# Kernel optimization log

Hardware: AMD Instinct MI355X
Metric: run time of the kernel (lower is better)

## Reference

```python
import jax, jax.numpy as jnp
import numpy as np

B, C, H, W = 8, 256, 48, 48

def setup_inputs() -> dict:
    key = jax.random.key(0)
    ks = jax.random.split(key, 8)
    s = 1.0 / np.sqrt(C)  # conv2d default init scale (uniform fan_in)
    x = jax.random.normal(ks[0], (B, C, H, W), dtype=jnp.float32)
    y = jax.random.normal(ks[1], (B, C, H, W), dtype=jnp.float32)
    Wq = jax.random.uniform(ks[2], (C, C), jnp.float32, -s, s)
    bq = jax.random.uniform(ks[3], (C,), jnp.float32, -s, s)
    Wk = jax.random.uniform(ks[4], (C, C), jnp.float32, -s, s)
    bk = jax.random.uniform(ks[5], (C,), jnp.float32, -s, s)
    Wv = jax.random.uniform(ks[6], (C, C), jnp.float32, -s, s)
    bv = jax.random.uniform(ks[7], (C,), jnp.float32, -s, s)
    return {"x": x, "y": y, "Wq": Wq, "bq": bq, "Wk": Wk, "bk": bk, "Wv": Wv, "bv": bv}

def reference(x, y, Wq, bq, Wk, bk, Wv, bv):
    b, c, h, w = x.shape
    n = h * w
    # [B,C,H,W] -> tokens [B,N,C]
    xt = x.reshape(b, c, n).transpose(0, 2, 1)
    yt = y.reshape(b, c, n).transpose(0, 2, 1)
    # 1x1 convs == per-token linear projections
    q = xt @ Wq.T + bq  # [B,N,C]
    k = yt @ Wk.T + bk  # [B,N,C]
    v = yt @ Wv.T + bv  # [B,N,C]
    # unscaled QK^T softmax (module applies no 1/sqrt(d) scaling)
    scores = jnp.einsum('bnc,bmc->bnm', q, k)  # [B,N,N]
    attn = jax.nn.softmax(scores, axis=-1)
    out = jnp.einsum('bnm,bmc->bnc', attn, v)  # [B,N,C]
    return out.transpose(0, 2, 1).reshape(b, c, h, w)
```

## Files before the change

### kernel.cpp

```cpp
#include <hip/hip_runtime.h>
#include <stdint.h>

#define Bb 8
#define Cc 256
#define Nn 2304
#define PQT 36
#define QTILES 36
#define KSPLIT 2
#define TPS 36
#define L2E 1.44269504088896f
#define DEFER_THR 8.0f

#define AS1 __attribute__((address_space(1)))
#define AS3 __attribute__((address_space(3)))

typedef unsigned short u16;
typedef unsigned int u32;
typedef _Float16 h16;
typedef h16  h16x8 __attribute__((ext_vector_type(8)));
typedef h16  h16x2 __attribute__((ext_vector_type(2)));
typedef u16  u16x8 __attribute__((ext_vector_type(8)));
typedef u32  u32x4 __attribute__((ext_vector_type(4)));
typedef float f32x4 __attribute__((ext_vector_type(4)));
typedef float f32x2 __attribute__((ext_vector_type(2)));

static __device__ __forceinline__ u16 f2h(float f) {
  return __builtin_bit_cast(u16, (h16)f);
}
static __device__ __forceinline__ h16x8 ash(u16x8 v) {
  return __builtin_bit_cast(h16x8, v);
}
static __device__ __forceinline__ f32x4 mfma16(u16x8 a, u16x8 b, f32x4 c) {
  return __builtin_amdgcn_mfma_f32_16x16x32_f16(ash(a), ash(b), c, 0, 0, 0);
}
static __device__ __forceinline__ u32 pkf16(float a, float b) {
  return __builtin_bit_cast(u32, __builtin_amdgcn_cvt_pkrtz(a, b));
}

__global__ void prep_kernel(const float* __restrict__ Wq,
                            const float* __restrict__ Wk,
                            const float* __restrict__ Wv,
                            u16* __restrict__ Wf)
{
  const int tid = blockIdx.x * 256 + threadIdx.x;
  const int m   = tid >> 13;
  const int off = (tid & 8191) * 8;
  const float* src = (m == 0) ? Wq : (m == 1) ? Wk : Wv;
  const f32x4 a = *(const f32x4*)(src + off);
  const f32x4 c = *(const f32x4*)(src + off + 4);
  u16x8 o;
#pragma unroll
  for (int j = 0; j < 4; ++j) { o[j] = f2h(a[j]); o[j + 4] = f2h(c[j]); }
  *(u16x8*)(Wf + (size_t)m * 65536 + off) = o;
}

__global__ __launch_bounds__(256, 4) void proj_kernel(
    const float* __restrict__ x, const float* __restrict__ y,
    const u16* __restrict__ Wf,
    const float* __restrict__ bq, const float* __restrict__ bk,
    const float* __restrict__ bv,
    u16* __restrict__ Qf, u16* __restrict__ Kf, u16* __restrict__ Vf)
{
  __shared__ u16 sW[32 * 256];
  const int t    = threadIdx.x;
  const int b    = blockIdx.x;
  const int q0   = blockIdx.y * 64;
  const int z    = blockIdx.z;
  const int lane = t & 63;
  const int w    = t >> 6;
  const int quad = lane >> 4;
  const int l15  = lane & 15;

  const u16* WZ = Wf + (size_t)z * 65536;

  const float* src = (z == 0) ? x : y;
  const int tok = q0 + w * 16 + l15;
  u16x8 af[8];
#pragma unroll
  for (int kc = 0; kc < 8; ++kc) {
    const float* p = src + ((size_t)b * Cc + kc * 32 + quad * 8) * Nn + tok;
    float v[8];
#pragma unroll
    for (int j = 0; j < 8; ++j) v[j] = p[(size_t)j * Nn];
#pragma unroll
    for (int j = 0; j < 8; ++j) af[kc][j] = f2h(v[j]);
  }

  f32x4 acc[16];
#pragma unroll
  for (int i = 0; i < 16; ++i) acc[i] = (f32x4){0.f, 0.f, 0.f, 0.f};

#pragma unroll 1
  for (int rg = 0; rg < 8; ++rg) {
    __syncthreads();
#pragma unroll
    for (int it = 0; it < 4; ++it) {
      const int id = it * 256 + t;
      const int row = id >> 5, gch = id & 31;
      const u16x8 v = *(const u16x8*)(WZ + (size_t)(rg * 32 + row) * 256 + gch * 8);
      *(u16x8*)(sW + row * 256 + ((gch ^ (row & 7)) << 3)) = v;
    }
    __syncthreads();
    if (z < 2) {
#pragma unroll
      for (int cbl = 0; cbl < 2; ++cbl) {
        const int rl = cbl * 16 + l15;
        f32x4 a = acc[rg * 2 + cbl];
#pragma unroll
        for (int kc = 0; kc < 8; ++kc) {
          const u16x8 bf = *(const u16x8*)(sW + rl * 256 + (((kc * 4 + quad) ^ (rl & 7)) << 3));
          a = mfma16(af[kc], bf, a);
        }
        acc[rg * 2 + cbl] = a;
      }
    } else {
#pragma unroll
      for (int mt = 0; mt < 2; ++mt) {
        const int rl = mt * 16 + l15;
        f32x4 a = acc[rg * 2 + mt];
#pragma unroll
        for (int kc = 0; kc < 8; ++kc) {
          const u16x8 wfr = *(const u16x8*)(sW + rl * 256 + (((kc * 4 + quad) ^ (rl & 7)) << 3));
          a = mfma16(wfr, af[kc], a);
        }
        acc[rg * 2 + mt] = a;
      }
    }
  }

  if (z < 2) {
    const float* bias = (z == 0) ? bq : bk;
    u16* O = (z == 0) ? Qf : Kf;
#pragma unroll
    for (int cb = 0; cb < 16; ++cb) {
      const int co = cb * 16 + l15;
      const float bs = bias[co];
      const size_t base = ((size_t)b * Nn + q0 + w * 16 + quad * 4) * Cc + co;
#pragma unroll
      for (int r = 0; r < 4; ++r)
        O[base + (size_t)r * Cc] = f2h(acc[cb][r] + bs);
    }
  } else {
#pragma unroll
    for (int cb = 0; cb < 16; ++cb) {
      const int crow = cb * 16 + quad * 4;
#pragma unroll
      for (int r = 0; r < 4; ++r)
        Vf[((size_t)b * Cc + crow + r) * Nn + q0 + w * 16 + l15] =
            f2h(acc[cb][r] + bv[crow + r]);
    }
  }
}

__global__ __launch_bounds__(256, 3) void attn_kernel(
    const u16* __restrict__ Qf, const u16* __restrict__ Kf,
    const u16* __restrict__ Vf, float* __restrict__ Opart,
    float* __restrict__ Ml)
{
  __shared__ u16 sK[32 * 256];
  __shared__ u16 sV[256 * 32];
  const int t    = threadIdx.x;
  const int b    = blockIdx.x;
  const int q0   = blockIdx.y * 64;
  const int sp   = blockIdx.z;
  const int lane = t & 63;
  const int w    = t >> 6;
  const int quad = lane >> 4;
  const int l15  = lane & 15;

  u16x8 qf[8];
  {
    const size_t qrow = ((size_t)b * Nn + q0 + w * 16 + l15) * Cc;
#pragma unroll
    for (int kc = 0; kc < 8; ++kc)
      qf[kc] = *(const u16x8*)(Qf + qrow + kc * 32 + quad * 8);
  }

  f32x4 o[16];
#pragma unroll
  for (int i = 0; i < 16; ++i) o[i] = (f32x4){0.f, 0.f, 0.f, 0.f};
  float mrow = -3e38f;
  float lrow = 0.f;

  const u16* Kb = Kf + (size_t)b * Nn * Cc;
  const u16* Vb = Vf + (size_t)b * Cc * Nn;

  const int rbase = 2 * w + (lane >> 5);
  const int kcol  = ((lane & 31) ^ rbase) << 3;
  const int rb2 = rbase >> 2, rb3 = rbase & 3;
  int koff[4];
#pragma unroll
  for (int it = 0; it < 4; ++it) {
    const int key = (((rb2 + 2 * it) & 3) << 3) + rb3 + ((it >> 1) << 2);
    koff[it] = key * Cc + kcol;
  }
  const u16* Kt = Kb + (size_t)(sp * TPS * 32) * Cc;
  const int cV   = w * 16 + (lane >> 2);
  const int vcol = ((lane & 3) ^ ((cV >> 1) & 3)) << 3;
  const u16* vp0 = Vb + (size_t)cV * Nn + sp * TPS * 32 + vcol;

  auto stage = [&](int kb) {
#pragma unroll
    for (int it = 0; it < 4; ++it) {
      __builtin_amdgcn_global_load_lds(
          (const AS1 void*)(Kt + (size_t)kb * 32 * Cc + koff[it]),
          (AS3 void*)&sK[(w + 4 * it) * 512], 16, 0, 0);
      __builtin_amdgcn_global_load_lds(
          (const AS1 void*)(vp0 + kb * 32 + (size_t)it * 64 * Nn),
          (AS3 void*)&sV[(w + 4 * it) * 512], 16, 0, 0);
    }
  };

  stage(0);

#pragma unroll 1
  for (int kb = 0; kb < TPS; ++kb) {
    __builtin_amdgcn_s_waitcnt(0x0F70);
    __syncthreads();

    f32x4 s0 = {0.f, 0.f, 0.f, 0.f}, s1 = s0;
#pragma unroll
    for (int kc = 0; kc < 8; ++kc) {
      const int ch = ((kc * 4 + quad) ^ (l15 & 7)) << 3;
      const u16x8 k0 = *(const u16x8*)(sK + l15 * 256 + ch);
      const u16x8 k1 = *(const u16x8*)(sK + (16 + l15) * 256 + ch);
      s0 = mfma16(k0, qf[kc], s0);
      s1 = mfma16(k1, qf[kc], s1);
    }

    float mloc = fmaxf(fmaxf(fmaxf(s0[0], s0[1]), fmaxf(s0[2], s0[3])),
                       fmaxf(fmaxf(s1[0], s1[1]), fmaxf(s1[2], s1[3])));
    mloc = fmaxf(mloc, __shfl_xor(mloc, 16, 64));
    mloc = fmaxf(mloc, __shfl_xor(mloc, 32, 64));
    const bool need = mloc > mrow + DEFER_THR;
    const float mn  = need ? mloc : mrow;
    const float al  = need ? exp2f((mrow - mn) * L2E) : 1.f;
    mrow = mn;

    float p0[4], p1[4];
    float sum = 0.f;
#pragma unroll
    for (int r = 0; r < 4; ++r) {
      p0[r] = exp2f((s0[r] - mn) * L2E);
      p1[r] = exp2f((s1[r] - mn) * L2E);
      sum += p0[r] + p1[r];
    }
    sum += __shfl_xor(sum, 16, 64);
    sum += __shfl_xor(sum, 32, 64);
    lrow = lrow * al + sum;

    if (__any(need)) {
#pragma unroll
      for (int i = 0; i < 16; ++i) {
#pragma unroll
        for (int r = 0; r < 4; ++r) o[i][r] *= al;
      }
    }

    u32x4 pw;
    pw[0] = pkf16(p0[0], p0[1]);
    pw[1] = pkf16(p0[2], p0[3]);
    pw[2] = pkf16(p1[0], p1[1]);
    pw[3] = pkf16(p1[2], p1[3]);
    const u16x8 pf = __builtin_bit_cast(u16x8, pw);

#pragma unroll
    for (int cb = 0; cb < 16; ++cb) {
      const int c = cb * 16 + l15;
      const u16x8 vf = *(const u16x8*)(sV + c * 32 + ((quad ^ ((c >> 1) & 3)) << 3));
      o[cb] = mfma16(vf, pf, o[cb]);
    }

    __syncthreads();
    if (kb + 1 < TPS) stage(kb + 1);
  }

  float* Ob = Opart + ((size_t)sp * Bb + b) * (size_t)Cc * Nn;
  const int qn = q0 + w * 16 + l15;
#pragma unroll
  for (int cb = 0; cb < 16; ++cb) {
#pragma unroll
    for (int r = 0; r < 4; ++r)
      Ob[(size_t)(cb * 16 + quad * 4 + r) * Nn + qn] = o[cb][r];
  }
  if (lane < 16) {
    float* mlb = Ml + ((size_t)sp * Bb + b) * (size_t)Nn * 2;
    *(f32x2*)(mlb + (size_t)qn * 2) = (f32x2){mrow, lrow};
  }
}

__global__ void merge_kernel(const float* __restrict__ Opart,
                             const float* __restrict__ Ml,
                             float* __restrict__ out)
{
  const int idx = blockIdx.x * 256 + threadIdx.x;
  const int n4 = idx % 576;
  const int bc = idx / 576;
  const int b  = bc >> 8;
  const size_t o0off = (size_t)bc * Nn + n4 * 4;
  const size_t ostride = (size_t)Bb * Cc * Nn;

  f32x4 ov[KSPLIT];
  float mv[KSPLIT][4], lv[KSPLIT][4];
#pragma unroll
  for (int s = 0; s < KSPLIT; ++s) {
    ov[s] = *(const f32x4*)(Opart + o0off + (size_t)s * ostride);
    const float* ml = Ml + ((size_t)s * Bb + b) * (size_t)Nn * 2 + n4 * 8;
    const f32x4 u0 = *(const f32x4*)ml;
    const f32x4 u1 = *(const f32x4*)(ml + 4);
#pragma unroll
    for (int j = 0; j < 4; ++j) {
      mv[s][j] = (j < 2) ? u0[j * 2]     : u1[(j - 2) * 2];
      lv[s][j] = (j < 2) ? u0[j * 2 + 1] : u1[(j - 2) * 2 + 1];
    }
  }

  f32x4 r;
#pragma unroll
  for (int j = 0; j < 4; ++j) {
    float m = mv[0][j];
#pragma unroll
    for (int s = 1; s < KSPLIT; ++s) m = fmaxf(m, mv[s][j]);
    float num = 0.f, den = 0.f;
#pragma unroll
    for (int s = 0; s < KSPLIT; ++s) {
      const float ws = exp2f((mv[s][j] - m) * L2E);
      num += ov[s][j] * ws;
      den += lv[s][j] * ws;
    }
    r[j] = num / den;
  }
  *(f32x4*)(out + o0off) = r;
}

extern "C" void kernel_launch(void* const* d_in, const int* in_sizes, int n_in,
                              void* d_out, int out_size, void* d_ws, size_t ws_size,
                              hipStream_t stream) {
  const float* x  = (const float*)d_in[0];
  const float* y  = (const float*)d_in[1];
  const float* Wq = (const float*)d_in[2];
  const float* bq = (const float*)d_in[3];
  const float* Wk = (const float*)d_in[4];
  const float* bk = (const float*)d_in[5];
  const float* Wv = (const float*)d_in[6];
  const float* bv = (const float*)d_in[7];
  float* out = (float*)d_out;

  const size_t NC = (size_t)Bb * Nn * Cc;
  u16* Qf = (u16*)d_ws;
  u16* Kf = Qf + NC;
  u16* Vf = Kf + NC;
  u16* Wf = Vf + NC;
  float* Opart = (float*)(Wf + 3 * 65536);
  float* Ml    = Opart + (size_t)KSPLIT * NC;

  hipLaunchKernelGGL(prep_kernel, dim3(96), dim3(256), 0, stream,
                     Wq, Wk, Wv, Wf);
  hipLaunchKernelGGL(proj_kernel, dim3(Bb, PQT, 3), dim3(256), 0, stream,
                     x, y, Wf, bq, bk, bv, Qf, Kf, Vf);
  hipLaunchKernelGGL(attn_kernel, dim3(Bb, QTILES, KSPLIT), dim3(256), 0, stream,
                     Qf, Kf, Vf, Opart, Ml);
  hipLaunchKernelGGL(merge_kernel, dim3(4608), dim3(256), 0, stream,
                     Opart, Ml, out);
}
```

Measured before the change: 237.4 us.

## Double query rows per wave, store fp16 normalized partials, fold weight prep into projection

The attention kernel now processes 32 query rows per wave, two 16-row groups that share each K/V shared-memory fragment. This doubles reuse of the staged K/V tiles at the cost of more registers and occupancy 2. The key split goes from 2 to 3 with 24 tiles each, and the partial outputs are normalized and stored as fp16 to halve merge traffic, with some precision risk. The separate weight-conversion kernel is removed: the projection kernel converts fp32 weights on the fly, and the K and V projections are fused into one block so the y activations are loaded once.

Result: slower. 262.9 us (+10.7%).

```diff
diff --git a/kernel.cpp b/kernel.cpp
--- a/kernel.cpp
+++ b/kernel.cpp
@@ -5,9 +5,9 @@
 #define Cc 256
 #define Nn 2304
 #define PQT 36
-#define QTILES 36
-#define KSPLIT 2
-#define TPS 36
+#define QT 18
+#define KSPLIT 3
+#define TPS 24
 #define L2E 1.44269504088896f
 #define DEFER_THR 8.0f
 
@@ -18,8 +18,8 @@
 typedef unsigned int u32;
 typedef _Float16 h16;
 typedef h16  h16x8 __attribute__((ext_vector_type(8)));
-typedef h16  h16x2 __attribute__((ext_vector_type(2)));
 typedef u16  u16x8 __attribute__((ext_vector_type(8)));
+typedef u16  u16x4 __attribute__((ext_vector_type(4)));
 typedef u32  u32x4 __attribute__((ext_vector_type(4)));
 typedef float f32x4 __attribute__((ext_vector_type(4)));
 typedef float f32x2 __attribute__((ext_vector_type(2)));
@@ -27,6 +27,9 @@
 static __device__ __forceinline__ u16 f2h(float f) {
   return __builtin_bit_cast(u16, (h16)f);
 }
+static __device__ __forceinline__ float h2f(u16 v) {
+  return (float)__builtin_bit_cast(h16, v);
+}
 static __device__ __forceinline__ h16x8 ash(u16x8 v) {
   return __builtin_bit_cast(h16x8, v);
 }
@@ -37,26 +40,10 @@
   return __builtin_bit_cast(u32, __builtin_amdgcn_cvt_pkrtz(a, b));
 }
 
-__global__ void prep_kernel(const float* __restrict__ Wq,
-                            const float* __restrict__ Wk,
-                            const float* __restrict__ Wv,
-                            u16* __restrict__ Wf)
-{
-  const int tid = blockIdx.x * 256 + threadIdx.x;
-  const int m   = tid >> 13;
-  const int off = (tid & 8191) * 8;
-  const float* src = (m == 0) ? Wq : (m == 1) ? Wk : Wv;
-  const f32x4 a = *(const f32x4*)(src + off);
-  const f32x4 c = *(const f32x4*)(src + off + 4);
-  u16x8 o;
-#pragma unroll
-  for (int j = 0; j < 4; ++j) { o[j] = f2h(a[j]); o[j + 4] = f2h(c[j]); }
-  *(u16x8*)(Wf + (size_t)m * 65536 + off) = o;
-}
-
-__global__ __launch_bounds__(256, 4) void proj_kernel(
+__global__ __launch_bounds__(256, 3) void proj_kernel(
     const float* __restrict__ x, const float* __restrict__ y,
-    const u16* __restrict__ Wf,
+    const float* __restrict__ Wq, const float* __restrict__ Wk,
+    const float* __restrict__ Wv,
     const float* __restrict__ bq, const float* __restrict__ bk,
     const float* __restrict__ bv,
     u16* __restrict__ Qf, u16* __restrict__ Kf, u16* __restrict__ Vf)
@@ -71,8 +58,6 @@
   const int quad = lane >> 4;
   const int l15  = lane & 15;
 
-  const u16* WZ = Wf + (size_t)z * 65536;
-
   const float* src = (z == 0) ? x : y;
   const int tok = q0 + w * 16 + l15;
   u16x8 af[8];
@@ -86,101 +71,117 @@
     for (int j = 0; j < 8; ++j) af[kc][j] = f2h(v[j]);
   }
 
-  f32x4 acc[16];
-#pragma unroll
-  for (int i = 0; i < 16; ++i) acc[i] = (f32x4){0.f, 0.f, 0.f, 0.f};
-
+  const int npass = z + 1;
 #pragma unroll 1
-  for (int rg = 0; rg < 8; ++rg) {
-    __syncthreads();
-#pragma unroll
-    for (int it = 0; it < 4; ++it) {
-      const int id = it * 256 + t;
-      const int row = id >> 5, gch = id & 31;
-      const u16x8 v = *(const u16x8*)(WZ + (size_t)(rg * 32 + row) * 256 + gch * 8);
-      *(u16x8*)(sW + row * 256 + ((gch ^ (row & 7)) << 3)) = v;
-    }
-    __syncthreads();
-    if (z < 2) {
-#pragma unroll
-      for (int cbl = 0; cbl < 2; ++cbl) {
-        const int rl = cbl * 16 + l15;
-        f32x4 a = acc[rg * 2 + cbl];
-#pragma unroll
-        for (int kc = 0; kc < 8; ++kc) {
-          const u16x8 bf = *(const u16x8*)(sW + rl * 256 + (((kc * 4 + quad) ^ (rl & 7)) << 3));
-          a = mfma16(af[kc], bf, a);
+  for (int pass = 0; pass < npass; ++pass) {
+    const float* W32 = (z == 0) ? Wq : (pass == 0 ? Wk : Wv);
+    const bool vpass = (z == 1) && (pass == 1);
+
+    f32x4 acc[16];
+#pragma unroll
+    for (int i = 0; i < 16; ++i) acc[i] = (f32x4){0.f, 0.f, 0.f, 0.f};
+
+#pragma unroll 1
+    for (int rg = 0; rg < 8; ++rg) {
+      __syncthreads();
+#pragma unroll
+      for (int it = 0; it < 4; ++it) {
+        const int id = it * 256 + t;
+        const int row = id >> 5, gch = id & 31;
+        const float* wp = W32 + (size_t)(rg * 32 + row) * 256 + gch * 8;
+        const f32x4 a = *(const f32x4*)wp;
+        const f32x4 c2 = *(const f32x4*)(wp + 4);
+        u16x8 ov;
+#pragma unroll
+        for (int j = 0; j < 4; ++j) { ov[j] = f2h(a[j]); ov[j + 4] = f2h(c2[j]); }
+        *(u16x8*)(sW + row * 256 + ((gch ^ (row & 7)) << 3)) = ov;
+      }
+      __syncthreads();
+      if (!vpass) {
+#pragma unroll
+        for (int cbl = 0; cbl < 2; ++cbl) {
+          const int rl = cbl * 16 + l15;
+          f32x4 a = acc[rg * 2 + cbl];
+#pragma unroll
+          for (int kc = 0; kc < 8; ++kc) {
+            const u16x8 bf = *(const u16x8*)(sW + rl * 256 + (((kc * 4 + quad) ^ (rl & 7)) << 3));
+            a = mfma16(af[kc], bf, a);
+          }
+          acc[rg * 2 + cbl] = a;
         }
-        acc[rg * 2 + cbl] = a;
+      } else {
+#pragma unroll
+        for (int mt = 0; mt < 2; ++mt) {
+          const int rl = mt * 16 + l15;
+          f32x4 a = acc[rg * 2 + mt];
+#pragma unroll
+          for (int kc = 0; kc < 8; ++kc) {
+            const u16x8 wfr = *(const u16x8*)(sW + rl * 256 + (((kc * 4 + quad) ^ (rl & 7)) << 3));
+            a = mfma16(wfr, af[kc], a);
+          }
+          acc[rg * 2 + mt] = a;
+        }
+      }
+    }
+
+    if (!vpass) {
+      const float* bias = (z == 0) ? bq : bk;
+      u16* O = (z == 0) ? Qf : Kf;
+#pragma unroll
+      for (int cb = 0; cb < 16; ++cb) {
+        const int co = cb * 16 + l15;
+        const float bs = bias[co];
+        const size_t base = ((size_t)b * Nn + q0 + w * 16 + quad * 4) * Cc + co;
+#pragma unroll
+        for (int r = 0; r < 4; ++r)
+          O[base + (size_t)r * Cc] = f2h(acc[cb][r] + bs);
       }
     } else {
 #pragma unroll
-      for (int mt = 0; mt < 2; ++mt) {
-        const int rl = mt * 16 + l15;
-        f32x4 a = acc[rg * 2 + mt];
-#pragma unroll
-        for (int kc = 0; kc < 8; ++kc) {
-          const u16x8 wfr = *(const u16x8*)(sW + rl * 256 + (((kc * 4 + quad) ^ (rl & 7)) << 3));
-          a = mfma16(wfr, af[kc], a);
-        }
-        acc[rg * 2 + mt] = a;
-      }
-    }
-  }
-
-  if (z < 2) {
-    const float* bias = (z == 0) ? bq : bk;
-    u16* O = (z == 0) ? Qf : Kf;
-#pragma unroll
-    for (int cb = 0; cb < 16; ++cb) {
-      const int co = cb * 16 + l15;
-      const float bs = bias[co];
-      const size_t base = ((size_t)b * Nn + q0 + w * 16 + quad * 4) * Cc + co;
-#pragma unroll
-      for (int r = 0; r < 4; ++r)
-        O[base + (size_t)r * Cc] = f2h(acc[cb][r] + bs);
-    }
-  } else {
-#pragma unroll
-    for (int cb = 0; cb < 16; ++cb) {
-      const int crow = cb * 16 + quad * 4;
-#pragma unroll
-      for (int r = 0; r < 4; ++r)
-        Vf[((size_t)b * Cc + crow + r) * Nn + q0 + w * 16 + l15] =
-            f2h(acc[cb][r] + bv[crow + r]);
-    }
-  }
-}
-
-__global__ __launch_bounds__(256, 3) void attn_kernel(
+      for (int cb = 0; cb < 16; ++cb) {
+        const int crow = cb * 16 + quad * 4;
+#pragma unroll
+        for (int r = 0; r < 4; ++r)
+          Vf[((size_t)b * Cc + crow + r) * Nn + q0 + w * 16 + l15] =
+              f2h(acc[cb][r] + bv[crow + r]);
+      }
+    }
+  }
+}
+
+__global__ __launch_bounds__(256, 2) void attn_kernel(
     const u16* __restrict__ Qf, const u16* __restrict__ Kf,
-    const u16* __restrict__ Vf, float* __restrict__ Opart,
+    const u16* __restrict__ Vf, u16* __restrict__ OpH,
     float* __restrict__ Ml)
 {
   __shared__ u16 sK[32 * 256];
   __shared__ u16 sV[256 * 32];
   const int t    = threadIdx.x;
   const int b    = blockIdx.x;
-  const int q0   = blockIdx.y * 64;
+  const int q0   = blockIdx.y * 128;
   const int sp   = blockIdx.z;
   const int lane = t & 63;
   const int w    = t >> 6;
   const int quad = lane >> 4;
   const int l15  = lane & 15;
-
-  u16x8 qf[8];
-  {
-    const size_t qrow = ((size_t)b * Nn + q0 + w * 16 + l15) * Cc;
+  const int wq0  = q0 + w * 32;
+
+  u16x8 qf[2][8];
+#pragma unroll
+  for (int g = 0; g < 2; ++g) {
+    const size_t qrow = ((size_t)b * Nn + wq0 + g * 16 + l15) * Cc;
 #pragma unroll
     for (int kc = 0; kc < 8; ++kc)
-      qf[kc] = *(const u16x8*)(Qf + qrow + kc * 32 + quad * 8);
-  }
-
-  f32x4 o[16];
-#pragma unroll
-  for (int i = 0; i < 16; ++i) o[i] = (f32x4){0.f, 0.f, 0.f, 0.f};
-  float mrow = -3e38f;
-  float lrow = 0.f;
+      qf[g][kc] = *(const u16x8*)(Qf + qrow + kc * 32 + quad * 8);
+  }
+
+  f32x4 o[2][16];
+#pragma unroll
+  for (int g = 0; g < 2; ++g)
+#pragma unroll
+    for (int i = 0; i < 16; ++i) o[g][i] = (f32x4){0.f, 0.f, 0.f, 0.f};
+  float mrow[2] = {-3e38f, -3e38f};
+  float lrow[2] = {0.f, 0.f};
 
   const u16* Kb = Kf + (size_t)b * Nn * Cc;
   const u16* Vb = Vf + (size_t)b * Cc * Nn;
@@ -213,83 +214,108 @@
 
   stage(0);
 
+  const int vbase = l15 * 32 + ((quad ^ ((l15 >> 1) & 3)) << 3);
+
 #pragma unroll 1
   for (int kb = 0; kb < TPS; ++kb) {
     __builtin_amdgcn_s_waitcnt(0x0F70);
     __syncthreads();
 
-    f32x4 s0 = {0.f, 0.f, 0.f, 0.f}, s1 = s0;
+    f32x4 s[2][2];
+    s[0][0] = (f32x4){0.f, 0.f, 0.f, 0.f}; s[0][1] = s[0][0];
+    s[1][0] = s[0][0];                      s[1][1] = s[0][0];
 #pragma unroll
     for (int kc = 0; kc < 8; ++kc) {
       const int ch = ((kc * 4 + quad) ^ (l15 & 7)) << 3;
       const u16x8 k0 = *(const u16x8*)(sK + l15 * 256 + ch);
       const u16x8 k1 = *(const u16x8*)(sK + (16 + l15) * 256 + ch);
-      s0 = mfma16(k0, qf[kc], s0);
-      s1 = mfma16(k1, qf[kc], s1);
-    }
-
-    float mloc = fmaxf(fmaxf(fmaxf(s0[0], s0[1]), fmaxf(s0[2], s0[3])),
-                       fmaxf(fmaxf(s1[0], s1[1]), fmaxf(s1[2], s1[3])));
-    mloc = fmaxf(mloc, __shfl_xor(mloc, 16, 64));
-    mloc = fmaxf(mloc, __shfl_xor(mloc, 32, 64));
-    const bool need = mloc > mrow + DEFER_THR;
-    const float mn  = need ? mloc : mrow;
-    const float al  = need ? exp2f((mrow - mn) * L2E) : 1.f;
-    mrow = mn;
-
-    float p0[4], p1[4];
-    float sum = 0.f;
-#pragma unroll
-    for (int r = 0; r < 4; ++r) {
-      p0[r] = exp2f((s0[r] - mn) * L2E);
-      p1[r] = exp2f((s1[r] - mn) * L2E);
-      sum += p0[r] + p1[r];
-    }
-    sum += __shfl_xor(sum, 16, 64);
-    sum += __shfl_xor(sum, 32, 64);
-    lrow = lrow * al + sum;
-
-    if (__any(need)) {
+      s[0][0] = mfma16(k0, qf[0][kc], s[0][0]);
+      s[0][1] = mfma16(k1, qf[0][kc], s[0][1]);
+      s[1][0] = mfma16(k0, qf[1][kc], s[1][0]);
+      s[1][1] = mfma16(k1, qf[1][kc], s[1][1]);
+    }
+
+    u16x8 pf[2];
+    float al[2];
+    int needany = 0;
+#pragma unroll
+    for (int g = 0; g < 2; ++g) {
+      float mloc = fmaxf(
+          fmaxf(fmaxf(s[g][0][0], s[g][0][1]), fmaxf(s[g][0][2], s[g][0][3])),
+          fmaxf(fmaxf(s[g][1][0], s[g][1][1]), fmaxf(s[g][1][2], s[g][1][3])));
+      mloc = fmaxf(mloc, __shfl_xor(mloc, 16, 64));
+      mloc = fmaxf(mloc, __shfl_xor(mloc, 32, 64));
+      const bool need = mloc > mrow[g] + DEFER_THR;
+      const float mn  = need ? mloc : mrow[g];
+      al[g] = need ? exp2f((mrow[g] - mn) * L2E) : 1.f;
+      mrow[g] = mn;
+      needany |= (int)need;
+
+      float p[8];
+      float sum = 0.f;
+#pragma unroll
+      for (int r = 0; r < 4; ++r) {
+        p[r]     = exp2f((s[g][0][r] - mn) * L2E);
+        p[4 + r] = exp2f((s[g][1][r] - mn) * L2E);
+        sum += p[r] + p[4 + r];
+      }
+      sum += __shfl_xor(sum, 16, 64);
+      sum += __shfl_xor(sum, 32, 64);
+      lrow[g] = lrow[g] * al[g] + sum;
+
+      u32x4 pw;
+      pw[0] = pkf16(p[0], p[1]);
+      pw[1] = pkf16(p[2], p[3]);
+      pw[2] = pkf16(p[4], p[5]);
+      pw[3] = pkf16(p[6], p[7]);
+      pf[g] = __builtin_bit_cast(u16x8, pw);
+    }
+
+    if (__any(needany)) {
 #pragma unroll
       for (int i = 0; i < 16; ++i) {
 #pragma unroll
-        for (int r = 0; r < 4; ++r) o[i][r] *= al;
-      }
-    }
-
-    u32x4 pw;
-    pw[0] = pkf16(p0[0], p0[1]);
-    pw[1] = pkf16(p0[2], p0[3]);
-    pw[2] = pkf16(p1[0], p1[1]);
-    pw[3] = pkf16(p1[2], p1[3]);
-    const u16x8 pf = __builtin_bit_cast(u16x8, pw);
+        for (int r = 0; r < 4; ++r) {
+          o[0][i][r] *= al[0];
+          o[1][i][r] *= al[1];
+        }
+      }
+    }
 
 #pragma unroll
     for (int cb = 0; cb < 16; ++cb) {
-      const int c = cb * 16 + l15;
-      const u16x8 vf = *(const u16x8*)(sV + c * 32 + ((quad ^ ((c >> 1) & 3)) << 3));
-      o[cb] = mfma16(vf, pf, o[cb]);
+      const u16x8 vf = *(const u16x8*)(sV + cb * 512 + vbase);
+      o[0][cb] = mfma16(vf, pf[0], o[0][cb]);
+      o[1][cb] = mfma16(vf, pf[1], o[1][cb]);
     }
 
     __syncthreads();
     if (kb + 1 < TPS) stage(kb + 1);
   }
 
-  float* Ob = Opart + ((size_t)sp * Bb + b) * (size_t)Cc * Nn;
-  const int qn = q0 + w * 16 + l15;
-#pragma unroll
-  for (int cb = 0; cb < 16; ++cb) {
-#pragma unroll
-    for (int r = 0; r < 4; ++r)
-      Ob[(size_t)(cb * 16 + quad * 4 + r) * Nn + qn] = o[cb][r];
+  u16* Ob = OpH + ((size_t)sp * Bb + b) * (size_t)Cc * Nn;
+#pragma unroll
+  for (int g = 0; g < 2; ++g) {
+    const float inv = 1.f / lrow[g];
+    const int qn = wq0 + g * 16 + l15;
+#pragma unroll
+    for (int cb = 0; cb < 16; ++cb) {
+#pragma unroll
+      for (int r = 0; r < 4; ++r)
+        Ob[(size_t)(cb * 16 + quad * 4 + r) * Nn + qn] = f2h(o[g][cb][r] * inv);
+    }
   }
   if (lane < 16) {
     float* mlb = Ml + ((size_t)sp * Bb + b) * (size_t)Nn * 2;
-    *(f32x2*)(mlb + (size_t)qn * 2) = (f32x2){mrow, lrow};
-  }
-}
-
-__global__ void merge_kernel(const float* __restrict__ Opart,
+#pragma unroll
+    for (int g = 0; g < 2; ++g) {
+      const int qn = wq0 + g * 16 + l15;
+      *(f32x2*)(mlb + (size_t)qn * 2) = (f32x2){mrow[g], lrow[g]};
+    }
+  }
+}
+
+__global__ void merge_kernel(const u16* __restrict__ OpH,
                              const float* __restrict__ Ml,
                              float* __restrict__ out)
 {
@@ -297,14 +323,14 @@
   const int n4 = idx % 576;
   const int bc = idx / 576;
   const int b  = bc >> 8;
-  const size_t o0off = (size_t)bc * Nn + n4 * 4;
-  const size_t ostride = (size_t)Bb * Cc * Nn;
-
-  f32x4 ov[KSPLIT];
-  float mv[KSPLIT][4], lv[KSPLIT][4];
+  const size_t obase = (size_t)bc * Nn + n4 * 4;
+
+  float oh[KSPLIT][4], mv[KSPLIT][4], lv[KSPLIT][4];
 #pragma unroll
   for (int s = 0; s < KSPLIT; ++s) {
-    ov[s] = *(const f32x4*)(Opart + o0off + (size_t)s * ostride);
+    const u16x4 hv = *(const u16x4*)(OpH + ((size_t)s * Bb * Cc + bc) * Nn + n4 * 4);
+#pragma unroll
+    for (int j = 0; j < 4; ++j) oh[s][j] = h2f(hv[j]);
     const float* ml = Ml + ((size_t)s * Bb + b) * (size_t)Nn * 2 + n4 * 8;
     const f32x4 u0 = *(const f32x4*)ml;
     const f32x4 u1 = *(const f32x4*)(ml + 4);
@@ -324,13 +350,13 @@
     float num = 0.f, den = 0.f;
 #pragma unroll
     for (int s = 0; s < KSPLIT; ++s) {
-      const float ws = exp2f((mv[s][j] - m) * L2E);
-      num += ov[s][j] * ws;
-      den += lv[s][j] * ws;
+      const float ws = lv[s][j] * exp2f((mv[s][j] - m) * L2E);
+      num += oh[s][j] * ws;
+      den += ws;
     }
     r[j] = num / den;
   }
-  *(f32x4*)(out + o0off) = r;
+  *(f32x4*)(out + obase) = r;
 }
 
 extern "C" void kernel_launch(void* const* d_in, const int* in_sizes, int n_in,
@@ -350,16 +376,13 @@
   u16* Qf = (u16*)d_ws;
   u16* Kf = Qf + NC;
   u16* Vf = Kf + NC;
-  u16* Wf = Vf + NC;
-  float* Opart = (float*)(Wf + 3 * 65536);
-  float* Ml    = Opart + (size_t)KSPLIT * NC;
-
-  hipLaunchKernelGGL(prep_kernel, dim3(96), dim3(256), 0, stream,
-                     Wq, Wk, Wv, Wf);
-  hipLaunchKernelGGL(proj_kernel, dim3(Bb, PQT, 3), dim3(256), 0, stream,
-                     x, y, Wf, bq, bk, bv, Qf, Kf, Vf);
-  hipLaunchKernelGGL(attn_kernel, dim3(Bb, QTILES, KSPLIT), dim3(256), 0, stream,
-                     Qf, Kf, Vf, Opart, Ml);
+  u16* OpH = Vf + NC;
+  float* Ml = (float*)(OpH + (size_t)KSPLIT * NC);
+
+  hipLaunchKernelGGL(proj_kernel, dim3(Bb, PQT, 2), dim3(256), 0, stream,
+                     x, y, Wq, Wk, Wv, bq, bk, bv, Qf, Kf, Vf);
+  hipLaunchKernelGGL(attn_kernel, dim3(Bb, QT, KSPLIT), dim3(256), 0, stream,
+                     Qf, Kf, Vf, OpH, Ml);
   hipLaunchKernelGGL(merge_kernel, dim3(4608), dim3(256), 0, stream,
-                     Opart, Ml, out);
-}
+                     OpH, Ml, out);
+}
```
